# Kernel tuning notes

Hardware: AMD Instinct MI355X
Metric: run time of the kernel (lower is better)

## Reference

```python
import jax, jax.numpy as jnp
import numpy as np
from jax import lax


def _conv(x, W):
    # NCHW conv, stride 1, SAME padding (padding = kernel//2 in original)
    return lax.conv_general_dilated(x, W, (1, 1), 'SAME',
                                    dimension_numbers=('NCHW', 'OIHW', 'NCHW'))


def _cconv(zr, zi, Wr, Wi, br, bi):
    # complex conv: (zr + i*zi) * (Wr + i*Wi)
    yr = _conv(zr, Wr) - _conv(zi, Wi) + br[None, :, None, None]
    yi = _conv(zr, Wi) + _conv(zi, Wr) + bi[None, :, None, None]
    return yr, yi


def setup_inputs() -> dict:
    key = jax.random.key(0)
    B, C, H, W = 16, 128, 64, 64        # C = 128 total = 64 real + 64 imag channels
    half = C // 2                        # 64 complex channels
    kin = (C + C) // 2                   # (input+hidden)/2 complex input channels = 128
    K = 3
    ks = jax.random.split(key, 20)
    inp = {
        'x':      jax.random.normal(ks[0], (B, C, H, W), jnp.float32),
        'h_prev': jax.random.normal(ks[1], (B, C, H, W), jnp.float32),
        'c_prev': jax.random.normal(ks[2], (B, C, H, W), jnp.float32),
    }
    i = 3
    for g in ('i', 'f', 'o', 'c'):
        inp['Wr_' + g] = jax.random.normal(ks[i], (half, kin, K, K), jnp.float32) * 0.05; i += 1
        inp['Wi_' + g] = jax.random.normal(ks[i], (half, kin, K, K), jnp.float32) * 0.05; i += 1
        inp['br_' + g] = jax.random.normal(ks[i], (half,), jnp.float32) * 0.05; i += 1
        inp['bi_' + g] = jax.random.normal(ks[i], (half,), jnp.float32) * 0.05; i += 1
    return inp


def reference(x, h_prev, c_prev,
              Wr_i, Wi_i, br_i, bi_i,
              Wr_f, Wi_f, br_f, bi_f,
              Wr_o, Wi_o, br_o, bi_o,
              Wr_c, Wi_c, br_c, bi_c):
    C = x.shape[1]
    h = C // 2
    xr, xi = x[:, :h], x[:, h:]
    hr, hi = h_prev[:, :h], h_prev[:, h:]
    cr, ci = c_prev[:, :h], c_prev[:, h:]

    zr = jnp.concatenate([xr, hr], axis=1)   # real part of combined
    zi = jnp.concatenate([xi, hi], axis=1)   # imag part of combined

    # gates: complex conv then split sigmoid / tanh (applied per component)
    i_r, i_i = map(jax.nn.sigmoid, _cconv(zr, zi, Wr_i, Wi_i, br_i, bi_i))
    # f gate conv output is computed but unused in final update (original bug keeps x as f)
    o_r, o_i = map(jax.nn.sigmoid, _cconv(zr, zi, Wr_o, Wi_o, br_o, bi_o))
    ct_r, ct_i = map(jnp.tanh, _cconv(zr, zi, Wr_c, Wi_c, br_c, bi_c))

    # faithful to original: f_r/f_i taken from x, not from conv_f output
    c_new_r = xr * cr - xi * ci + i_r * ct_r - i_i * ct_i
    c_new_i = xr * ci + xi * cr + i_r * ct_i + i_i * ct_r

    t_r = jnp.tanh(c_new_r)
    t_i = jnp.tanh(c_new_i)
    h_new = jnp.concatenate([o_r * t_r - o_i * t_i, o_r * t_i + o_i * t_r], axis=1)
    c_new = jnp.concatenate([c_new_r, c_new_i], axis=1)
    return h_new, c_new
```

## Files before the change

kernel.cpp:

```cpp
#include <hip/hip_runtime.h>
#include <hip/hip_bf16.h>


typedef __attribute__((ext_vector_type(8))) short short8;
typedef __attribute__((ext_vector_type(4))) float floatx4;
typedef __attribute__((ext_vector_type(4))) float float4v;

#define MTOT   65536
#define HSIZE  8388608
#define ZP_ELEMS (16 * 66 * 66 * 256)

__device__ __forceinline__ short f2bf(float f) {
  __hip_bfloat16 h = __float2bfloat16(f);
  return *reinterpret_cast<short*>(&h);
}

__device__ __forceinline__ void gload16(const short* g, void* lds) {
  __builtin_amdgcn_global_load_lds(
      (__attribute__((address_space(1))) void*)(g),
      (__attribute__((address_space(3))) void*)(lds), 16, 0, 0);
}

__global__ __launch_bounds__(256) void halo_zero_kernel(short* __restrict__ Zp) {
  int t = blockIdx.x * 256 + threadIdx.x;
  int s   = t & 31;
  int pix = t >> 5;
  int b = pix / 260;
  int r = pix - b * 260;
  int yp, xp;
  if (r < 66)       { yp = 0;               xp = r; }
  else if (r < 132) { yp = 65;              xp = r - 66; }
  else { int r2 = r - 132; yp = 1 + (r2 >> 1); xp = (r2 & 1) * 65; }
  short8 z;
#pragma unroll
  for (int q = 0; q < 8; ++q) z[q] = 0;
  *(short8*)(Zp + (((b * 66 + yp) * 66 + xp) * 256 + s * 8)) = z;
}

__global__ __launch_bounds__(256) void pack_z_kernel(
    const float* __restrict__ xs, const float* __restrict__ hs,
    short* __restrict__ Zp) {
  __shared__ short tile[64 * 72];
  int bid = blockIdx.x;
  int y      = bid & 63;
  int half   = (bid >> 6) & 1;
  int srcSel = (bid >> 7) & 1;
  int b      = bid >> 8;
  const float* src = srcSel ? hs : xs;
  int chBase  = half * 64;
  int cinBase = half * 128 + srcSel * 64;
  int t = threadIdx.x;
  int x4 = t & 15, chq = t >> 4;
#pragma unroll
  for (int p = 0; p < 4; ++p) {
    int ch = p * 16 + chq;
    float4v f = *(const float4v*)(src + (size_t)(b * 128 + chBase + ch) * 4096 + y * 64 + x4 * 4);
#pragma unroll
    for (int e = 0; e < 4; ++e)
      tile[(x4 * 4 + e) * 72 + ch] = f2bf(f[e]);
  }
  __syncthreads();
  int x = t >> 2, seg = t & 3;
  short8 v0 = *(const short8*)(tile + x * 72 + seg * 16);
  short8 v1 = *(const short8*)(tile + x * 72 + seg * 16 + 8);
  size_t outp = ((size_t)(b * 66 + y + 1) * 66 + x + 1) * 256 + cinBase + seg * 16;
  *(short8*)(Zp + outp)     = v0;
  *(short8*)(Zp + outp + 8) = v1;
}

__global__ __launch_bounds__(256) void pack_w_kernel(
    const float* __restrict__ Wr_i, const float* __restrict__ Wi_i,
    const float* __restrict__ Wr_o, const float* __restrict__ Wi_o,
    const float* __restrict__ Wr_c, const float* __restrict__ Wi_c,
    const float* __restrict__ br_i, const float* __restrict__ bi_i,
    const float* __restrict__ br_o, const float* __restrict__ bi_o,
    const float* __restrict__ br_c, const float* __restrict__ bi_c,
    short* __restrict__ Wp, float* __restrict__ bias) {
  int g = blockIdx.x * 256 + threadIdx.x;
  if (g >= 384 * 9 * 256) return;
  int cin = g & 255;
  int tap = (g >> 8) % 9;
  int n   = g / (256 * 9);
  int part = n >> 6, ch = n & 63;
  const float *Wr, *Wi;
  if (part < 2)      { Wr = Wr_i; Wi = Wi_i; }
  else if (part < 4) { Wr = Wr_o; Wi = Wi_o; }
  else               { Wr = Wr_c; Wi = Wi_c; }
  int im = part & 1;
  int ci = cin & 127;
  int second = cin >> 7;
  const float* src = im ? (second ? Wr : Wi) : (second ? Wi : Wr);
  float f = src[(ch * 128 + ci) * 9 + tap];
  if (!im && second) f = -f;
  Wp[(n * 9 + tap) * 256 + cin] = f2bf(f);
  if (g < 384) {
    int p2 = g >> 6, c2 = g & 63;
    const float* bs = (p2 == 0) ? br_i : (p2 == 1) ? bi_i : (p2 == 2) ? br_o
                    : (p2 == 3) ? bi_o : (p2 == 4) ? br_c : bi_c;
    bias[g] = bs[c2];
  }
}

__global__ __launch_bounds__(256, 3) void conv_gemm(
    const short* __restrict__ Z, const short* __restrict__ Wp,
    const float* __restrict__ bias, __hip_bfloat16* __restrict__ gates) {
  __shared__ short8 As[1024];
  __shared__ short8 Bs[1056];

  const int tid = threadIdx.x;
  const int wv = tid >> 6, lane = tid & 63;
  const int l15 = lane & 15, l4 = lane >> 4;
  const int m0 = blockIdx.x * 128;
  const int n0 = blockIdx.y * 128;
  const int b  = m0 >> 12;
  const int y0 = (m0 >> 6) & 63;
  const int wch = (wv & 1) * 64;
  const int r2w = wv >> 1;

  floatx4 acc[4][4];
#pragma unroll
  for (int i = 0; i < 4; ++i)
#pragma unroll
    for (int j = 0; j < 4; ++j)
#pragma unroll
      for (int r = 0; r < 4; ++r) acc[i][j][r] = 0.f;

  for (int dy = -1; dy <= 1; ++dy) {
    for (int c0 = 0; c0 < 256; c0 += 64) {
#pragma unroll
      for (int it = 0; it < 5; ++it) {
        int idx = tid + it * 256;
        if (idx < 1056) {
          int r2  = (idx >= 528) ? 1 : 0;
          int rem = idx - r2 * 528;
          int col = rem >> 3, p = rem & 7;
          int g   = p ^ (col & 7);
          int ygl = b * 66 + y0 + dy + 1 + r2;
          gload16(Z + ((size_t)(ygl * 66 + col) * 256 + c0 + g * 8),
                  (void*)(Bs + (it * 256 + wv * 64)));
        }
      }
      for (int dx = -1; dx <= 1; ++dx) {
        int tap = (dy + 1) * 3 + (dx + 1);
#pragma unroll
        for (int it = 0; it < 4; ++it) {
          int idx = tid + it * 256;
          int row = idx >> 3, p = idx & 7;
          int g   = p ^ (row & 7);
          gload16(Wp + ((size_t)((n0 + row) * 9 + tap) * 256 + c0 + g * 8),
                  (void*)(As + (it * 256 + wv * 64)));
        }
        __syncthreads();
#pragma unroll
        for (int kk = 0; kk < 2; ++kk) {
          int kg = kk * 4 + l4;
          short8 a[4], bf[4];
#pragma unroll
          for (int i = 0; i < 4; ++i) {
            int row = wch + i * 16 + l15;
            a[i] = As[row * 8 + (kg ^ (row & 7))];
          }
#pragma unroll
          for (int j = 0; j < 4; ++j) {
            int col = j * 16 + l15 + dx + 1;
            bf[j] = Bs[r2w * 528 + col * 8 + (kg ^ (col & 7))];
          }
#pragma unroll
          for (int i = 0; i < 4; ++i)
#pragma unroll
            for (int j = 0; j < 4; ++j)
              acc[i][j] = __builtin_amdgcn_mfma_f32_16x16x32_bf16(a[i], bf[j], acc[i][j], 0, 0, 0);
        }
        __syncthreads();
      }
    }
  }
#pragma unroll
  for (int i = 0; i < 4; ++i)
#pragma unroll
    for (int j = 0; j < 4; ++j)
#pragma unroll
      for (int r = 0; r < 4; ++r) {
        int ch = n0 + wch + i * 16 + l4 * 4 + r;
        int px = m0 + r2w * 64 + j * 16 + l15;
        gates[(size_t)ch * MTOT + px] = __float2bfloat16(acc[i][j][r] + bias[ch]);
      }
}

__device__ __forceinline__ float fsig(float v) { return 1.f / (1.f + __expf(-v)); }
__device__ __forceinline__ float ftanh(float v) {
  float e = __expf(2.f * v);
  return 1.f - 2.f / (e + 1.f);
}

__global__ __launch_bounds__(256) void epilogue_kernel(
    const __hip_bfloat16* __restrict__ gates,
    const float* __restrict__ x,
    const float* __restrict__ c_prev,
    float* __restrict__ out) {
  int g = blockIdx.x * 256 + threadIdx.x;
  int m  = g & (MTOT - 1);
  int ch = g >> 16;
  int b = m >> 12, sp = m & 4095;
  float yri = __bfloat162float(gates[(size_t)(0 * 64 + ch) * MTOT + m]);
  float yii = __bfloat162float(gates[(size_t)(1 * 64 + ch) * MTOT + m]);
  float yro = __bfloat162float(gates[(size_t)(2 * 64 + ch) * MTOT + m]);
  float yio = __bfloat162float(gates[(size_t)(3 * 64 + ch) * MTOT + m]);
  float yrc = __bfloat162float(gates[(size_t)(4 * 64 + ch) * MTOT + m]);
  float yic = __bfloat162float(gates[(size_t)(5 * 64 + ch) * MTOT + m]);
  float i_r = fsig(yri), i_i = fsig(yii);
  float o_r = fsig(yro), o_i = fsig(yio);
  float ct_r = ftanh(yrc), ct_i = ftanh(yic);
  int base = (b * 128 + ch) * 4096 + sp;
  float xr = x[base];
  float xi = x[base + 64 * 4096];
  float cr = c_prev[base];
  float ci = c_prev[base + 64 * 4096];
  float cnr = xr * cr - xi * ci + i_r * ct_r - i_i * ct_i;
  float cni = xr * ci + xi * cr + i_r * ct_i + i_i * ct_r;
  float tr = ftanh(cnr), ti = ftanh(cni);
  out[base]                     = o_r * tr - o_i * ti;
  out[base + 64 * 4096]         = o_r * ti + o_i * tr;
  out[HSIZE + base]             = cnr;
  out[HSIZE + base + 64 * 4096] = cni;
}

extern "C" void kernel_launch(void* const* d_in, const int* in_sizes, int n_in,
                              void* d_out, int out_size, void* d_ws, size_t ws_size,
                              hipStream_t stream) {
  const float* x = (const float*)d_in[0];
  const float* h = (const float*)d_in[1];

  char* ws = (char*)d_ws;
  short* Zp   = (short*)ws;
  short* Wp   = (short*)(ws + 35684352);
  float* bias = (float*)(ws + 37453824);
  __hip_bfloat16* gates = (__hip_bfloat16*)(ws + 37455360);

  halo_zero_kernel<<<520, 256, 0, stream>>>(Zp);
  pack_z_kernel<<<4096, 256, 0, stream>>>(x, h, Zp);
  pack_w_kernel<<<3456, 256, 0, stream>>>(
      (const float*)d_in[3], (const float*)d_in[4],
      (const float*)d_in[11], (const float*)d_in[12],
      (const float*)d_in[15], (const float*)d_in[16],
      (const float*)d_in[5], (const float*)d_in[6],
      (const float*)d_in[13], (const float*)d_in[14],
      (const float*)d_in[17], (const float*)d_in[18],
      Wp, bias);
  conv_gemm<<<dim3(512, 3), 256, 0, stream>>>(Zp, Wp, bias, gates);
  epilogue_kernel<<<16384, 256, 0, stream>>>(
      gates, (const float*)d_in[0], (const float*)d_in[2],
      (float*)d_out);
}
```

Before: 319.0 us.

## Fuse conv GEMM with LSTM epilogue, merge prep kernels, pipeline loads

Merges the three packing kernels into a single prep launch. Replaces the conv GEMM plus separate epilogue with one fused kernel in which each block computes all 384 gate channels for two image rows and applies the sigmoid/tanh cell update directly from LDS. This removes the bf16 gates round trip through global memory and one launch. The main loop is also restructured with double-buffered A/B tiles, explicit waitcnt and barrier scheduling, and raised priority around the MFMA blocks. In exchange there is higher register and LDS use, fewer blocks (512), and more complex manual synchronisation.

```diff
diff --git a/kernel.cpp b/kernel.cpp
--- a/kernel.cpp
+++ b/kernel.cpp
@@ -6,13 +6,16 @@
 typedef __attribute__((ext_vector_type(4))) float floatx4;
 typedef __attribute__((ext_vector_type(4))) float float4v;
 
-#define MTOT   65536
 #define HSIZE  8388608
-#define ZP_ELEMS (16 * 66 * 66 * 256)
 
 __device__ __forceinline__ short f2bf(float f) {
   __hip_bfloat16 h = __float2bfloat16(f);
   return *reinterpret_cast<short*>(&h);
+}
+
+__device__ __forceinline__ float bf2f(short s) {
+  unsigned u = ((unsigned)(unsigned short)s) << 16;
+  return __uint_as_float(u);
 }
 
 __device__ __forceinline__ void gload16(const short* g, void* lds) {
@@ -21,54 +24,9 @@
       (__attribute__((address_space(3))) void*)(lds), 16, 0, 0);
 }
 
-__global__ __launch_bounds__(256) void halo_zero_kernel(short* __restrict__ Zp) {
-  int t = blockIdx.x * 256 + threadIdx.x;
-  int s   = t & 31;
-  int pix = t >> 5;
-  int b = pix / 260;
-  int r = pix - b * 260;
-  int yp, xp;
-  if (r < 66)       { yp = 0;               xp = r; }
-  else if (r < 132) { yp = 65;              xp = r - 66; }
-  else { int r2 = r - 132; yp = 1 + (r2 >> 1); xp = (r2 & 1) * 65; }
-  short8 z;
-#pragma unroll
-  for (int q = 0; q < 8; ++q) z[q] = 0;
-  *(short8*)(Zp + (((b * 66 + yp) * 66 + xp) * 256 + s * 8)) = z;
-}
-
-__global__ __launch_bounds__(256) void pack_z_kernel(
+__global__ __launch_bounds__(256) void prep_kernel(
     const float* __restrict__ xs, const float* __restrict__ hs,
-    short* __restrict__ Zp) {
-  __shared__ short tile[64 * 72];
-  int bid = blockIdx.x;
-  int y      = bid & 63;
-  int half   = (bid >> 6) & 1;
-  int srcSel = (bid >> 7) & 1;
-  int b      = bid >> 8;
-  const float* src = srcSel ? hs : xs;
-  int chBase  = half * 64;
-  int cinBase = half * 128 + srcSel * 64;
-  int t = threadIdx.x;
-  int x4 = t & 15, chq = t >> 4;
-#pragma unroll
-  for (int p = 0; p < 4; ++p) {
-    int ch = p * 16 + chq;
-    float4v f = *(const float4v*)(src + (size_t)(b * 128 + chBase + ch) * 4096 + y * 64 + x4 * 4);
-#pragma unroll
-    for (int e = 0; e < 4; ++e)
-      tile[(x4 * 4 + e) * 72 + ch] = f2bf(f[e]);
-  }
-  __syncthreads();
-  int x = t >> 2, seg = t & 3;
-  short8 v0 = *(const short8*)(tile + x * 72 + seg * 16);
-  short8 v1 = *(const short8*)(tile + x * 72 + seg * 16 + 8);
-  size_t outp = ((size_t)(b * 66 + y + 1) * 66 + x + 1) * 256 + cinBase + seg * 16;
-  *(short8*)(Zp + outp)     = v0;
-  *(short8*)(Zp + outp + 8) = v1;
-}
-
-__global__ __launch_bounds__(256) void pack_w_kernel(
+    short* __restrict__ Zp,
     const float* __restrict__ Wr_i, const float* __restrict__ Wi_i,
     const float* __restrict__ Wr_o, const float* __restrict__ Wi_o,
     const float* __restrict__ Wr_c, const float* __restrict__ Wi_c,
@@ -76,115 +34,131 @@
     const float* __restrict__ br_o, const float* __restrict__ bi_o,
     const float* __restrict__ br_c, const float* __restrict__ bi_c,
     short* __restrict__ Wp, float* __restrict__ bias) {
-  int g = blockIdx.x * 256 + threadIdx.x;
-  if (g >= 384 * 9 * 256) return;
-  int cin = g & 255;
-  int tap = (g >> 8) % 9;
-  int n   = g / (256 * 9);
-  int part = n >> 6, ch = n & 63;
-  const float *Wr, *Wi;
-  if (part < 2)      { Wr = Wr_i; Wi = Wi_i; }
-  else if (part < 4) { Wr = Wr_o; Wi = Wi_o; }
-  else               { Wr = Wr_c; Wi = Wi_c; }
-  int im = part & 1;
-  int ci = cin & 127;
-  int second = cin >> 7;
-  const float* src = im ? (second ? Wr : Wi) : (second ? Wi : Wr);
-  float f = src[(ch * 128 + ci) * 9 + tap];
-  if (!im && second) f = -f;
-  Wp[(n * 9 + tap) * 256 + cin] = f2bf(f);
-  if (g < 384) {
-    int p2 = g >> 6, c2 = g & 63;
-    const float* bs = (p2 == 0) ? br_i : (p2 == 1) ? bi_i : (p2 == 2) ? br_o
-                    : (p2 == 3) ? bi_o : (p2 == 4) ? br_c : bi_c;
-    bias[g] = bs[c2];
-  }
-}
-
-__global__ __launch_bounds__(256, 3) void conv_gemm(
-    const short* __restrict__ Z, const short* __restrict__ Wp,
-    const float* __restrict__ bias, __hip_bfloat16* __restrict__ gates) {
-  __shared__ short8 As[1024];
-  __shared__ short8 Bs[1056];
-
-  const int tid = threadIdx.x;
-  const int wv = tid >> 6, lane = tid & 63;
-  const int l15 = lane & 15, l4 = lane >> 4;
-  const int m0 = blockIdx.x * 128;
-  const int n0 = blockIdx.y * 128;
-  const int b  = m0 >> 12;
-  const int y0 = (m0 >> 6) & 63;
-  const int wch = (wv & 1) * 64;
-  const int r2w = wv >> 1;
-
-  floatx4 acc[4][4];
-#pragma unroll
-  for (int i = 0; i < 4; ++i)
+  __shared__ short tile[64 * 72];
+  int blk = blockIdx.x;
+  int tid = threadIdx.x;
+
+  if (blk < 520) {
+    int t = blk * 256 + tid;
+    int s   = t & 31;
+    int pix = t >> 5;
+    int b = pix / 260;
+    int r = pix - b * 260;
+    int yp, xp;
+    if (r < 66)       { yp = 0;               xp = r; }
+    else if (r < 132) { yp = 65;              xp = r - 66; }
+    else { int r2 = r - 132; yp = 1 + (r2 >> 1); xp = (r2 & 1) * 65; }
+    short8 z;
+#pragma unroll
+    for (int q = 0; q < 8; ++q) z[q] = 0;
+    *(short8*)(Zp + (((b * 66 + yp) * 66 + xp) * 256 + s * 8)) = z;
+    return;
+  }
+
+  if (blk < 520 + 4096) {
+    int bid = blk - 520;
+    int y      = bid & 63;
+    int half   = (bid >> 6) & 1;
+    int srcSel = (bid >> 7) & 1;
+    int b      = bid >> 8;
+    const float* src = srcSel ? hs : xs;
+    int chBase  = half * 64;
+    int cinBase = half * 128 + srcSel * 64;
+    int x4 = tid & 15, chq = tid >> 4;
+#pragma unroll
+    for (int p = 0; p < 4; ++p) {
+      int ch = p * 16 + chq;
+      float4v f = *(const float4v*)(src + (size_t)(b * 128 + chBase + ch) * 4096 + y * 64 + x4 * 4);
+#pragma unroll
+      for (int e = 0; e < 4; ++e)
+        tile[(x4 * 4 + e) * 72 + ch] = f2bf(f[e]);
+    }
+    __syncthreads();
+    int x = tid >> 2, seg = tid & 3;
+    short8 v0 = *(const short8*)(tile + x * 72 + seg * 16);
+    short8 v1 = *(const short8*)(tile + x * 72 + seg * 16 + 8);
+    size_t outp = ((size_t)(b * 66 + y + 1) * 66 + x + 1) * 256 + cinBase + seg * 16;
+    *(short8*)(Zp + outp)     = v0;
+    *(short8*)(Zp + outp + 8) = v1;
+    return;
+  }
+
+  {
+    int g = (blk - 4616) * 256 + tid;
+    if (g >= 384 * 9 * 256) return;
+    int cin = g & 255;
+    int tap = (g >> 8) % 9;
+    int n   = g / (256 * 9);
+    int part = n >> 6, ch = n & 63;
+    const float *Wr, *Wi;
+    if (part < 2)      { Wr = Wr_i; Wi = Wi_i; }
+    else if (part < 4) { Wr = Wr_o; Wi = Wi_o; }
+    else               { Wr = Wr_c; Wi = Wi_c; }
+    int im = part & 1;
+    int ci = cin & 127;
+    int second = cin >> 7;
+    const float* src = im ? (second ? Wr : Wi) : (second ? Wi : Wr);
+    float f = src[(ch * 128 + ci) * 9 + tap];
+    if (!im && second) f = -f;
+    Wp[(n * 9 + tap) * 256 + cin] = f2bf(f);
+    if (g < 384) {
+      int p2 = g >> 6, c2 = g & 63;
+      const float* bs = (p2 == 0) ? br_i : (p2 == 1) ? bi_i : (p2 == 2) ? br_o
+                      : (p2 == 3) ? bi_o : (p2 == 4) ? br_c : bi_c;
+      bias[g] = bs[c2];
+    }
+  }
+}
+
+__device__ __forceinline__ void issueA(const short* __restrict__ Wp, int tapkc,
+                                       short8* dst, int tid, int wv) {
+#pragma unroll
+  for (int it = 0; it < 3; ++it) {
+    int idx = tid + it * 512;
+    int row = idx >> 2, p = idx & 3;
+    int g = p ^ (row & 3);
+    gload16(Wp + ((size_t)row * 2304 + tapkc + g * 8),
+            (void*)(dst + (it * 512 + wv * 64)));
+  }
+}
+
+__device__ __forceinline__ void issueBc(const short* __restrict__ Z, int zrow0,
+                                        int kcn32, int tapc, short8* dst,
+                                        int tid, int wv) {
+  int idx = tapc * 512 + tid;
+  int row = idx >> 8;
+  int rem = idx & 255;
+  int col = 1 + (rem >> 2);
+  int p   = idx & 3;
+  int g   = p ^ (col & 3);
+  int base = tapc * 512 + wv * 64;
+  int rowu = base >> 8;
+  gload16(Z + ((size_t)((zrow0 + row) * 66 + col) * 256 + kcn32 + g * 8),
+          (void*)(dst + (base + rowu * 8 + 4)));
+}
+
+template<int DYN, int DXN>
+__device__ __forceinline__ void readFrags(const short8* __restrict__ Ab,
+                                          const short8* __restrict__ Bb0,
+                                          short8 (&af)[6], short8 (&bf)[4],
+                                          int aBase, int wpx, int l15, int l4) {
+  const short8* Bb = Bb0 + (wpx + DYN) * 264;
+  int bb = (l15 + DXN) * 4 + (l4 ^ ((l15 + DXN) & 3));
+#pragma unroll
+  for (int i = 0; i < 6; ++i) af[i] = Ab[aBase + i * 64];
+#pragma unroll
+  for (int j = 0; j < 4; ++j) bf[j] = Bb[bb + j * 64];
+}
+
+__device__ __forceinline__ void mfma24(const short8 (&af)[6], const short8 (&bf)[4],
+                                       floatx4 (&acc)[6][4]) {
+  __builtin_amdgcn_s_setprio(1);
+#pragma unroll
+  for (int i = 0; i < 6; ++i)
 #pragma unroll
     for (int j = 0; j < 4; ++j)
-#pragma unroll
-      for (int r = 0; r < 4; ++r) acc[i][j][r] = 0.f;
-
-  for (int dy = -1; dy <= 1; ++dy) {
-    for (int c0 = 0; c0 < 256; c0 += 64) {
-#pragma unroll
-      for (int it = 0; it < 5; ++it) {
-        int idx = tid + it * 256;
-        if (idx < 1056) {
-          int r2  = (idx >= 528) ? 1 : 0;
-          int rem = idx - r2 * 528;
-          int col = rem >> 3, p = rem & 7;
-          int g   = p ^ (col & 7);
-          int ygl = b * 66 + y0 + dy + 1 + r2;
-          gload16(Z + ((size_t)(ygl * 66 + col) * 256 + c0 + g * 8),
-                  (void*)(Bs + (it * 256 + wv * 64)));
-        }
-      }
-      for (int dx = -1; dx <= 1; ++dx) {
-        int tap = (dy + 1) * 3 + (dx + 1);
-#pragma unroll
-        for (int it = 0; it < 4; ++it) {
-          int idx = tid + it * 256;
-          int row = idx >> 3, p = idx & 7;
-          int g   = p ^ (row & 7);
-          gload16(Wp + ((size_t)((n0 + row) * 9 + tap) * 256 + c0 + g * 8),
-                  (void*)(As + (it * 256 + wv * 64)));
-        }
-        __syncthreads();
-#pragma unroll
-        for (int kk = 0; kk < 2; ++kk) {
-          int kg = kk * 4 + l4;
-          short8 a[4], bf[4];
-#pragma unroll
-          for (int i = 0; i < 4; ++i) {
-            int row = wch + i * 16 + l15;
-            a[i] = As[row * 8 + (kg ^ (row & 7))];
-          }
-#pragma unroll
-          for (int j = 0; j < 4; ++j) {
-            int col = j * 16 + l15 + dx + 1;
-            bf[j] = Bs[r2w * 528 + col * 8 + (kg ^ (col & 7))];
-          }
-#pragma unroll
-          for (int i = 0; i < 4; ++i)
-#pragma unroll
-            for (int j = 0; j < 4; ++j)
-              acc[i][j] = __builtin_amdgcn_mfma_f32_16x16x32_bf16(a[i], bf[j], acc[i][j], 0, 0, 0);
-        }
-        __syncthreads();
-      }
-    }
-  }
-#pragma unroll
-  for (int i = 0; i < 4; ++i)
-#pragma unroll
-    for (int j = 0; j < 4; ++j)
-#pragma unroll
-      for (int r = 0; r < 4; ++r) {
-        int ch = n0 + wch + i * 16 + l4 * 4 + r;
-        int px = m0 + r2w * 64 + j * 16 + l15;
-        gates[(size_t)ch * MTOT + px] = __float2bfloat16(acc[i][j][r] + bias[ch]);
-      }
+      acc[i][j] = __builtin_amdgcn_mfma_f32_16x16x32_bf16(af[i], bf[j], acc[i][j], 0, 0, 0);
+  __builtin_amdgcn_s_setprio(0);
 }
 
 __device__ __forceinline__ float fsig(float v) { return 1.f / (1.f + __expf(-v)); }
@@ -193,53 +167,149 @@
   return 1.f - 2.f / (e + 1.f);
 }
 
-__global__ __launch_bounds__(256) void epilogue_kernel(
-    const __hip_bfloat16* __restrict__ gates,
-    const float* __restrict__ x,
-    const float* __restrict__ c_prev,
-    float* __restrict__ out) {
-  int g = blockIdx.x * 256 + threadIdx.x;
-  int m  = g & (MTOT - 1);
-  int ch = g >> 16;
-  int b = m >> 12, sp = m & 4095;
-  float yri = __bfloat162float(gates[(size_t)(0 * 64 + ch) * MTOT + m]);
-  float yii = __bfloat162float(gates[(size_t)(1 * 64 + ch) * MTOT + m]);
-  float yro = __bfloat162float(gates[(size_t)(2 * 64 + ch) * MTOT + m]);
-  float yio = __bfloat162float(gates[(size_t)(3 * 64 + ch) * MTOT + m]);
-  float yrc = __bfloat162float(gates[(size_t)(4 * 64 + ch) * MTOT + m]);
-  float yic = __bfloat162float(gates[(size_t)(5 * 64 + ch) * MTOT + m]);
-  float i_r = fsig(yri), i_i = fsig(yii);
-  float o_r = fsig(yro), o_i = fsig(yio);
-  float ct_r = ftanh(yrc), ct_i = ftanh(yic);
-  int base = (b * 128 + ch) * 4096 + sp;
-  float xr = x[base];
-  float xi = x[base + 64 * 4096];
-  float cr = c_prev[base];
-  float ci = c_prev[base + 64 * 4096];
-  float cnr = xr * cr - xi * ci + i_r * ct_r - i_i * ct_i;
-  float cni = xr * ci + xi * cr + i_r * ct_i + i_i * ct_r;
-  float tr = ftanh(cnr), ti = ftanh(cni);
-  out[base]                     = o_r * tr - o_i * ti;
-  out[base + 64 * 4096]         = o_r * ti + o_i * tr;
-  out[HSIZE + base]             = cnr;
-  out[HSIZE + base + 64 * 4096] = cni;
+__global__ __launch_bounds__(512, 2) void conv_fused(
+    const short* __restrict__ Z, const short* __restrict__ Wp,
+    const float* __restrict__ bias, const float* __restrict__ x,
+    const float* __restrict__ c_prev, float* __restrict__ out) {
+  __shared__ short8 As[2][1536];
+  __shared__ short8 Bs[2][1056];
+
+  const int tid = threadIdx.x;
+  const int wv = tid >> 6, lane = tid & 63;
+  const int l15 = lane & 15, l4 = lane >> 4;
+  const int wc4 = wv & 3;
+  const int wpx = wv >> 2;
+  const int pb = blockIdx.x;
+  const int b  = pb >> 5;
+  const int y0 = (pb & 31) * 2;
+  const int zrow0 = b * 66 + y0;
+
+  const int aBase = (wc4 * 96 + l15) * 4 + (l4 ^ (l15 & 3));
+
+  floatx4 acc[6][4];
+#pragma unroll
+  for (int i = 0; i < 6; ++i)
+#pragma unroll
+    for (int j = 0; j < 4; ++j)
+#pragma unroll
+      for (int r = 0; r < 4; ++r) acc[i][j][r] = 0.f;
+
+  short8 afA[6], bfA[4], afB[6], bfB[4];
+
+  if (tid < 64) {
+    int buf = tid >> 5, w = tid & 31;
+    int r = w >> 3, hi = (w >> 2) & 1, p = w & 3;
+    short8 z;
+#pragma unroll
+    for (int q = 0; q < 8; ++q) z[q] = 0;
+    Bs[buf][r * 264 + (hi ? 260 : 0) + p] = z;
+  }
+  issueA(Wp, 0, &As[0][0], tid, wv);
+  issueBc(Z, zrow0, 0, 0, &Bs[0][0], tid, wv);
+  issueBc(Z, zrow0, 0, 1, &Bs[0][0], tid, wv);
+  issueA(Wp, 256, &As[1][0], tid, wv);
+  __builtin_amdgcn_sched_barrier(0);
+  asm volatile("s_waitcnt vmcnt(3) lgkmcnt(0)" ::: "memory");
+  __builtin_amdgcn_sched_barrier(0);
+  __builtin_amdgcn_s_barrier();
+  __builtin_amdgcn_sched_barrier(0);
+  readFrags<0, 0>(&As[0][0], &Bs[0][0], afA, bfA, aBase, wpx, l15, l4);
+
+#define STEP(TAP, PE, KCV)                                                     \
+  {                                                                            \
+    constexpr int PS   = ((TAP) + (PE)) & 1;                                   \
+    constexpr int TAPN = ((TAP) + 1) % 9;                                      \
+    constexpr int PBN  = ((TAP) == 8) ? ((PE) ^ 1) : (PE);                     \
+    if constexpr ((TAP) == 1 || (TAP) == 2)                                    \
+      asm volatile("s_waitcnt vmcnt(1) lgkmcnt(0)" ::: "memory");              \
+    else                                                                       \
+      asm volatile("s_waitcnt vmcnt(0) lgkmcnt(0)" ::: "memory");              \
+    __builtin_amdgcn_sched_barrier(0);                                         \
+    __builtin_amdgcn_s_barrier();                                              \
+    __builtin_amdgcn_sched_barrier(0);                                         \
+    if constexpr (PS == 0)                                                     \
+      readFrags<TAPN / 3, TAPN % 3>(&As[1][0], &Bs[PBN][0], afB, bfB,          \
+                                    aBase, wpx, l15, l4);                      \
+    else                                                                       \
+      readFrags<TAPN / 3, TAPN % 3>(&As[0][0], &Bs[PBN][0], afA, bfA,          \
+                                    aBase, wpx, l15, l4);                      \
+    { const int kc2 = ((TAP) <= 6) ? (KCV) : (KCV) + 1;                        \
+      issueA(Wp, (((TAP) + 2) % 9) * 256 + kc2 * 32, &As[PS][0], tid, wv); }   \
+    if constexpr ((TAP) == 0 || (TAP) == 1)                                    \
+      issueBc(Z, zrow0, ((KCV) + 1) * 32, (TAP), &Bs[(PE) ^ 1][0], tid, wv);   \
+    if constexpr (PS == 0) mfma24(afA, bfA, acc);                              \
+    else                   mfma24(afB, bfB, acc);                              \
+  }
+
+  for (int kq = 0; kq < 4; ++kq) {
+    const int kE = kq * 2, kO = kE + 1;
+    STEP(0, 0, kE) STEP(1, 0, kE) STEP(2, 0, kE) STEP(3, 0, kE) STEP(4, 0, kE)
+    STEP(5, 0, kE) STEP(6, 0, kE) STEP(7, 0, kE) STEP(8, 0, kE)
+    STEP(0, 1, kO) STEP(1, 1, kO) STEP(2, 1, kO) STEP(3, 1, kO) STEP(4, 1, kO)
+    STEP(5, 1, kO) STEP(6, 1, kO) STEP(7, 1, kO) STEP(8, 1, kO)
+  }
+#undef STEP
+
+  asm volatile("s_waitcnt vmcnt(0) lgkmcnt(0)" ::: "memory");
+  __syncthreads();
+  short* Ex = (short*)&As[0][0];
+#pragma unroll
+  for (int l = 0; l < 2; ++l) {
+    if (wpx == l) {
+#pragma unroll
+      for (int i = 0; i < 6; ++i)
+#pragma unroll
+        for (int j = 0; j < 4; ++j)
+#pragma unroll
+          for (int rr = 0; rr < 4; ++rr) {
+            int ch = wc4 * 96 + i * 16 + l4 * 4 + rr;
+            int xx = j * 16 + l15;
+            Ex[ch * 64 + xx] = f2bf(acc[i][j][rr] + bias[ch]);
+          }
+    }
+    __syncthreads();
+    {
+      int xg = tid & 63, cg = tid >> 6;
+#pragma unroll
+      for (int k = 0; k < 8; ++k) {
+        int c = cg * 8 + k;
+        float yri = bf2f(Ex[(0 * 64 + c) * 64 + xg]);
+        float yii = bf2f(Ex[(1 * 64 + c) * 64 + xg]);
+        float yro = bf2f(Ex[(2 * 64 + c) * 64 + xg]);
+        float yio = bf2f(Ex[(3 * 64 + c) * 64 + xg]);
+        float yrc = bf2f(Ex[(4 * 64 + c) * 64 + xg]);
+        float yic = bf2f(Ex[(5 * 64 + c) * 64 + xg]);
+        float i_r = fsig(yri), i_i = fsig(yii);
+        float o_r = fsig(yro), o_i = fsig(yio);
+        float ct_r = ftanh(yrc), ct_i = ftanh(yic);
+        int base = (b * 128 + c) * 4096 + (y0 + l) * 64 + xg;
+        float xr = x[base];
+        float xi = x[base + 64 * 4096];
+        float cr = c_prev[base];
+        float ci = c_prev[base + 64 * 4096];
+        float cnr = xr * cr - xi * ci + i_r * ct_r - i_i * ct_i;
+        float cni = xr * ci + xi * cr + i_r * ct_i + i_i * ct_r;
+        float tr = ftanh(cnr), ti = ftanh(cni);
+        out[base]                     = o_r * tr - o_i * ti;
+        out[base + 64 * 4096]         = o_r * ti + o_i * tr;
+        out[HSIZE + base]             = cnr;
+        out[HSIZE + base + 64 * 4096] = cni;
+      }
+    }
+    __syncthreads();
+  }
 }
 
 extern "C" void kernel_launch(void* const* d_in, const int* in_sizes, int n_in,
                               void* d_out, int out_size, void* d_ws, size_t ws_size,
                               hipStream_t stream) {
-  const float* x = (const float*)d_in[0];
-  const float* h = (const float*)d_in[1];
-
   char* ws = (char*)d_ws;
   short* Zp   = (short*)ws;
   short* Wp   = (short*)(ws + 35684352);
   float* bias = (float*)(ws + 37453824);
-  __hip_bfloat16* gates = (__hip_bfloat16*)(ws + 37455360);
-
-  halo_zero_kernel<<<520, 256, 0, stream>>>(Zp);
-  pack_z_kernel<<<4096, 256, 0, stream>>>(x, h, Zp);
-  pack_w_kernel<<<3456, 256, 0, stream>>>(
+
+  prep_kernel<<<8072, 256, 0, stream>>>(
+      (const float*)d_in[0], (const float*)d_in[1], Zp,
       (const float*)d_in[3], (const float*)d_in[4],
       (const float*)d_in[11], (const float*)d_in[12],
       (const float*)d_in[15], (const float*)d_in[16],
@@ -247,8 +317,7 @@
       (const float*)d_in[13], (const float*)d_in[14],
       (const float*)d_in[17], (const float*)d_in[18],
       Wp, bias);
-  conv_gemm<<<dim3(512, 3), 256, 0, stream>>>(Zp, Wp, bias, gates);
-  epilogue_kernel<<<16384, 256, 0, stream>>>(
-      gates, (const float*)d_in[0], (const float*)d_in[2],
+  conv_fused<<<512, 512, 0, stream>>>(
+      Zp, Wp, bias, (const float*)d_in[0], (const float*)d_in[2],
       (float*)d_out);
 }
```

New measurement: 310.0 us. -2.8%, faster.
